# Optimization experiments

Hardware: AMD Instinct MI355X
Metric: run time of the kernel (lower is better)

Reference implementation:

```python
import jax, jax.numpy as jnp
import numpy as np

B, T, D = 2048, 200, 64
H1, H2, H3 = 256, 128, 64


def prelu(x, alpha):
    # keras PReLU default: alpha shaped like non-batch dims (T, units)
    return jnp.maximum(x, 0) + alpha * jnp.minimum(x, 0)


def setup_inputs() -> dict:
    key = jax.random.key(0)
    ks = jax.random.split(key, 12)
    q = jax.random.normal(ks[0], (B, 1, D), dtype=jnp.float32)
    k = jax.random.normal(ks[1], (B, T, D), dtype=jnp.float32)
    s1 = 1.0 / np.sqrt(4 * D)
    s2 = 1.0 / np.sqrt(H1)
    s3 = 1.0 / np.sqrt(H2)
    s4 = 1.0 / np.sqrt(H3)
    W1 = jax.random.normal(ks[2], (4 * D, H1), dtype=jnp.float32) * s1
    b1 = jnp.zeros((H1,), dtype=jnp.float32)
    a1 = jnp.full((T, H1), 0.25, dtype=jnp.float32)
    W2 = jax.random.normal(ks[3], (H1, H2), dtype=jnp.float32) * s2
    b2 = jnp.zeros((H2,), dtype=jnp.float32)
    a2 = jnp.full((T, H2), 0.25, dtype=jnp.float32)
    W3 = jax.random.normal(ks[4], (H2, H3), dtype=jnp.float32) * s3
    b3 = jnp.zeros((H3,), dtype=jnp.float32)
    a3 = jnp.full((T, H3), 0.25, dtype=jnp.float32)
    Wl = jax.random.normal(ks[5], (H3, 1), dtype=jnp.float32) * s4
    bl = jnp.zeros((1,), dtype=jnp.float32)
    return {"q": q, "k": k, "W1": W1, "b1": b1, "a1": a1,
            "W2": W2, "b2": b2, "a2": a2, "W3": W3, "b3": b3, "a3": a3,
            "Wl": Wl, "bl": bl}


def reference(q, k, W1, b1, a1, W2, b2, a2, W3, b3, a3, Wl, bl):
    # q: [B,1,D] broadcast over T; k: [B,T,D]
    qt = jnp.broadcast_to(q, k.shape)                     # [B,T,D] (tile)
    att_in = jnp.concatenate([qt, k, qt - k, qt * k], axis=-1)  # [B,T,4D]
    h = prelu(jnp.einsum('btf,fh->bth', att_in, W1) + b1, a1)   # [B,T,H1]
    h = prelu(jnp.einsum('btf,fh->bth', h, W2) + b2, a2)        # [B,T,H2]
    h = prelu(jnp.einsum('btf,fh->bth', h, W3) + b3, a3)        # [B,T,H3]
    score = (jnp.einsum('btf,fo->bto', h, Wl) + bl)[..., 0]     # [B,T]
    mask = k[:, :, 0] != 0
    score = jnp.where(mask, score, 0.0)
    out = jnp.einsum('bt,btd->bd', score, k)              # [B,D]
    return out
```

## Files before the change

### kernel.cpp

```cpp
#include <hip/hip_runtime.h>
#include <stdint.h>

#define BB 2048
#define TT 200
#define DD 64
#define FF 256
#define H1C 256
#define H2C 128
#define H3C 64

typedef __bf16 bf16x8 __attribute__((ext_vector_type(8)));
typedef float floatx16 __attribute__((ext_vector_type(16)));
typedef float f32x4 __attribute__((ext_vector_type(4)));
typedef uint32_t u32x4 __attribute__((ext_vector_type(4)));
typedef uint32_t u32x2 __attribute__((ext_vector_type(2)));
typedef unsigned short u16;
typedef u16 u16x8 __attribute__((ext_vector_type(8)));

__device__ inline u16 f2bf(float f) {
    uint32_t u = __builtin_bit_cast(uint32_t, f) + 0x8000u;
    return (u16)(u >> 16);
}
__device__ inline float bf2f(u16 h) {
    uint32_t u = ((uint32_t)h) << 16;
    return __builtin_bit_cast(float, u);
}
__device__ inline uint32_t pkbf(float lo, float hi) {
    uint32_t ul = __builtin_bit_cast(uint32_t, lo) + 0x8000u;
    uint32_t uh = __builtin_bit_cast(uint32_t, hi) + 0x8000u;
    return __builtin_amdgcn_perm(uh, ul, 0x07060302);
}

template<int K, int N>
__device__ inline void pack_w2_dev(const float* __restrict__ Wa, const float* __restrict__ Wb,
                                   float sgn, u16* __restrict__ out, int blk) {
    constexpr int NC = K / 16;
    int idx = blk * 256 + threadIdx.x;
    int j    = idx & 7;
    int lane = (idx >> 3) & 63;
    int rest = idx >> 9;
    int c  = rest % NC;
    int mt = rest / NC;
    int k = c * 16 + ((lane >> 5) << 3) + j;
    int n = mt * 32 + (lane & 31);
    out[idx] = f2bf(Wa[k * N + n] + sgn * Wb[k * N + n]);
}
template<int NTOT>
__device__ inline void pack_a_dev(const float* __restrict__ A, u16* __restrict__ out, int blk) {
    constexpr int MTOT = NTOT / 32;
    int idx = blk * 256 + threadIdx.x;
    int reg  = idx & 15;
    int lane = (idx >> 4) & 63;
    int rest = idx >> 10;
    int mt = rest % MTOT;
    int g  = rest / MTOT;
    int t  = (g >> 1) * 64 + (g & 1) * 32 + (lane & 31);
    int n  = mt * 32 + (reg & 3) + ((reg >> 2) << 3) + ((lane >> 5) << 2);
    out[idx] = (t < TT) ? f2bf(A[t * NTOT + n]) : (u16)0;
}

__global__ void pack_all(const float* __restrict__ W1, const float* __restrict__ W2,
                         const float* __restrict__ W3, const float* __restrict__ a1,
                         const float* __restrict__ a2, const float* __restrict__ a3,
                         u16* W1kdp, u16* W1pp, u16* W1qdp, u16* W2p, u16* W3p,
                         u16* A1p, u16* A2p, u16* A3p) {
    int blk = blockIdx.x;
    const float* W1q = W1;
    const float* W1k = W1 + 64 * H1C;
    const float* W1d = W1 + 128 * H1C;
    const float* W1p = W1 + 192 * H1C;
    if      (blk < 64)  pack_w2_dev<64, H1C>(W1k, W1d, -1.f, W1kdp, blk);
    else if (blk < 128) pack_w2_dev<64, H1C>(W1p, W1p,  0.f, W1pp,  blk - 64);
    else if (blk < 192) pack_w2_dev<64, H1C>(W1q, W1d,  1.f, W1qdp, blk - 128);
    else if (blk < 320) pack_w2_dev<H1C, H2C>(W2, W2,   0.f, W2p,   blk - 192);
    else if (blk < 352) pack_w2_dev<H2C, H3C>(W3, W3,   0.f, W3p,   blk - 320);
    else if (blk < 608) pack_a_dev<H1C>(a1, A1p, blk - 352);
    else if (blk < 736) pack_a_dev<H2C>(a2, A2p, blk - 608);
    else                pack_a_dev<H3C>(a3, A3p, blk - 736);
}

__device__ __attribute__((always_inline)) inline
void store_tile(u16* yrow, int S, const floatx16& acc, u16x8 av0, u16x8 av1) {
#pragma unroll
    for (int q = 0; q < 4; ++q) {
        float p[4];
#pragma unroll
        for (int i = 0; i < 4; ++i) {
            const int r = q * 4 + i;
            float v = acc[r];
            float al = bf2f(r < 8 ? av0[r] : av1[r - 8]);
            p[i] = fmaxf(v, 0.f) + al * fminf(v, 0.f);
        }
        u32x2 pw = { pkbf(p[0], p[1]), pkbf(p[2], p[3]) };
        *reinterpret_cast<u32x2*>(yrow + ((q ^ S) << 3)) = pw;
    }
}

__device__ inline void load_k4(const float* __restrict__ Kin, int b, int t, int c0,
                               f32x4* kk) {
    if (t < TT) {
        const f32x4* p = reinterpret_cast<const f32x4*>(Kin + ((size_t)b * TT + t) * DD + c0);
#pragma unroll
        for (int i = 0; i < 4; ++i) kk[i] = __builtin_nontemporal_load(p + i);
    } else {
#pragma unroll
        for (int i = 0; i < 4; ++i) kk[i] = f32x4{0.f, 0.f, 0.f, 0.f};
    }
}

__global__ __launch_bounds__(256, 2)
void attn_pool_kernel(const float* __restrict__ Q, const float* __restrict__ Kin,
                      const u16* __restrict__ W1kdp, const u16* __restrict__ W1pp,
                      const u16* __restrict__ W1qdp, const float* __restrict__ b1,
                      const u16* __restrict__ A1p,
                      const u16* __restrict__ W2p, const float* __restrict__ b2,
                      const u16* __restrict__ A2p,
                      const u16* __restrict__ W3p, const float* __restrict__ b3,
                      const u16* __restrict__ A3p,
                      const float* __restrict__ Wl, const float* __restrict__ bl,
                      float* __restrict__ Out) {
    __shared__ __align__(16) u16 k_sh[64 * 72];
    __shared__ __align__(16) u16 h1s[64 * 264];
    __shared__ __align__(16) u16 h2s[64 * 136];
    __shared__ float q_sh[64];
    __shared__ float k0_sh[64];
    __shared__ float fb1_sh[H1C];
    __shared__ float pool_red[4][64];

    const int tid  = threadIdx.x;
    const int lane = tid & 63;
    const int w    = tid >> 6;
    const int b    = blockIdx.x;
    const int tl   = lane & 31;
    const int hl   = lane >> 5;
    const int kq   = hl << 3;
    const int hsel = hl << 2;
    const int S    = (tl >> 3) & 1;
    const int r    = tid >> 2;
    const int c0   = (tid & 3) << 4;

    if (tid < 16) {
        reinterpret_cast<f32x4*>(q_sh)[tid] =
            reinterpret_cast<const f32x4*>(Q + (size_t)b * DD)[tid];
    }
    const float bl0 = bl[0];

    f32x4 kn[4];
    load_k4(Kin, b, r, c0, kn);
    __syncthreads();

    bf16x8 mf[2][4];
    {
#pragma unroll
        for (int s = 0; s < 2; ++s) {
            const int mt = w + 4 * s;
            const size_t fo = ((size_t)(mt * 4) * 64 + lane) * 8;
            floatx16 accb;
#pragma unroll
            for (int i = 0; i < 16; ++i) accb[i] = 0.f;
#pragma unroll
            for (int c = 0; c < 4; ++c) {
                u16x8 kd = *reinterpret_cast<const u16x8*>(W1kdp + fo + (size_t)c * 512);
                u16x8 pf = *reinterpret_cast<const u16x8*>(W1pp  + fo + (size_t)c * 512);
                bf16x8 qd = *reinterpret_cast<const bf16x8*>(W1qdp + fo + (size_t)c * 512);
                f32x4 qa = *reinterpret_cast<const f32x4*>(&q_sh[c * 16 + kq]);
                f32x4 qb = *reinterpret_cast<const f32x4*>(&q_sh[c * 16 + kq + 4]);
                u32x4 qpack = { pkbf(qa[0], qa[1]), pkbf(qa[2], qa[3]),
                                pkbf(qb[0], qb[1]), pkbf(qb[2], qb[3]) };
                bf16x8 qf = __builtin_bit_cast(bf16x8, qpack);
                accb = __builtin_amdgcn_mfma_f32_32x32x16_bf16(qd, qf, accb, 0, 0, 0);
                float mv[8];
#pragma unroll
                for (int j = 0; j < 4; ++j) mv[j]     = bf2f(kd[j])     + bf2f(pf[j])     * qa[j];
#pragma unroll
                for (int j = 0; j < 4; ++j) mv[4 + j] = bf2f(kd[4 + j]) + bf2f(pf[4 + j]) * qb[j];
                u32x4 mpack = { pkbf(mv[0], mv[1]), pkbf(mv[2], mv[3]),
                                pkbf(mv[4], mv[5]), pkbf(mv[6], mv[7]) };
                mf[s][c] = __builtin_bit_cast(bf16x8, mpack);
            }
            if (tl == 0) {
#pragma unroll
                for (int q = 0; q < 4; ++q) {
                    f32x4 bv = *reinterpret_cast<const f32x4*>(b1 + mt * 32 + q * 8 + hsel);
#pragma unroll
                    for (int i = 0; i < 4; ++i)
                        fb1_sh[mt * 32 + q * 8 + hsel + i] = accb[q * 4 + i] + bv[i];
                }
            }
        }
    }

    bf16x8 wf2[16];
    {
        const u16* p2 = W2p + (size_t)(w * 16) * 512 + lane * 8;
#pragma unroll
        for (int c = 0; c < 16; ++c)
            wf2[c] = *reinterpret_cast<const bf16x8*>(p2 + (size_t)c * 512);
    }
    const int mt3 = w & 1, tt3 = w >> 1;
    floatx16 bq2, bq3;
#pragma unroll
    for (int q = 0; q < 4; ++q) {
        f32x4 v2 = *reinterpret_cast<const f32x4*>(b2 + w * 32 + q * 8 + hsel);
        f32x4 v3 = *reinterpret_cast<const f32x4*>(b3 + mt3 * 32 + q * 8 + hsel);
#pragma unroll
        for (int i = 0; i < 4; ++i) { bq2[q * 4 + i] = v2[i]; bq3[q * 4 + i] = v3[i]; }
    }

    float pacc = 0.f;

#pragma unroll 1
    for (int mb = 0; mb < 4; ++mb) {
        const int t0 = mb * 64;

        {
            f32x4 kc[4] = { kn[0], kn[1], kn[2], kn[3] };
            if (mb < 3) load_k4(Kin, b, t0 + 64 + r, c0, kn);
            u32x4 ua = { pkbf(kc[0][0], kc[0][1]), pkbf(kc[0][2], kc[0][3]),
                         pkbf(kc[1][0], kc[1][1]), pkbf(kc[1][2], kc[1][3]) };
            u32x4 ub = { pkbf(kc[2][0], kc[2][1]), pkbf(kc[2][2], kc[2][3]),
                         pkbf(kc[3][0], kc[3][1]), pkbf(kc[3][2], kc[3][3]) };
            *reinterpret_cast<u32x4*>(k_sh + r * 72 + c0)     = ua;
            *reinterpret_cast<u32x4*>(k_sh + r * 72 + c0 + 8) = ub;
            if (c0 == 0) k0_sh[r] = kc[0][0];
        }
        __syncthreads();

#pragma unroll
        for (int s = 0; s < 2; ++s) {
            const int mt = w + 4 * s;
#pragma unroll
            for (int tt = 0; tt < 2; ++tt) {
                const u16* ap = A1p + (((size_t)((mb * 2 + tt) * 8 + mt) * 64 + lane) << 4);
                u16x8 av0 = *reinterpret_cast<const u16x8*>(ap);
                u16x8 av1 = *reinterpret_cast<const u16x8*>(ap + 8);
                floatx16 acc;
#pragma unroll
                for (int q = 0; q < 4; ++q) {
                    f32x4 bv = *reinterpret_cast<const f32x4*>(&fb1_sh[mt * 32 + q * 8 + hsel]);
#pragma unroll
                    for (int i = 0; i < 4; ++i) acc[q * 4 + i] = bv[i];
                }
                const u16* xb = k_sh + (tt * 32 + tl) * 72 + kq;
#pragma unroll
                for (int c = 0; c < 4; ++c)
                    acc = __builtin_amdgcn_mfma_f32_32x32x16_bf16(
                        mf[s][c], *reinterpret_cast<const bf16x8*>(xb + c * 16), acc, 0, 0, 0);
                store_tile(h1s + (tt * 32 + tl) * 264 + mt * 32 + hsel, S, acc, av0, av1);
            }
        }
        __syncthreads();

#pragma unroll
        for (int tt = 0; tt < 2; ++tt) {
            const u16* ap = A2p + (((size_t)((mb * 2 + tt) * 4 + w) * 64 + lane) << 4);
            u16x8 av0 = *reinterpret_cast<const u16x8*>(ap);
            u16x8 av1 = *reinterpret_cast<const u16x8*>(ap + 8);
            floatx16 acc = bq2;
            const u16* xb = h1s + (tt * 32 + tl) * 264 + ((hl ^ S) << 3);
#pragma unroll
            for (int c = 0; c < 16; ++c)
                acc = __builtin_amdgcn_mfma_f32_32x32x16_bf16(
                    wf2[c], *reinterpret_cast<const bf16x8*>(xb + c * 16), acc, 0, 0, 0);
            store_tile(h2s + (tt * 32 + tl) * 136 + w * 32 + hsel, S, acc, av0, av1);
        }
        __syncthreads();

        {
            const u16* ap = A3p + (((size_t)((mb * 2 + tt3) * 2 + mt3) * 64 + lane) << 4);
            u16x8 av0 = *reinterpret_cast<const u16x8*>(ap);
            u16x8 av1 = *reinterpret_cast<const u16x8*>(ap + 8);
            const u16* wp3 = W3p + (size_t)(mt3 * 8) * 512 + lane * 8;
            floatx16 acc = bq3;
            const u16* xb = h2s + (tt3 * 32 + tl) * 136 + ((hl ^ S) << 3);
#pragma unroll
            for (int c = 0; c < 8; ++c)
                acc = __builtin_amdgcn_mfma_f32_32x32x16_bf16(
                    *reinterpret_cast<const bf16x8*>(wp3 + (size_t)c * 512),
                    *reinterpret_cast<const bf16x8*>(xb + c * 16), acc, 0, 0, 0);
            store_tile(h1s + (tt3 * 32 + tl) * 264 + mt3 * 32 + hsel, S, acc, av0, av1);
        }
        __syncthreads();

        {
            const int sr  = tid >> 2;
            const int p   = tid & 3;
            const int Ssc = (sr >> 3) & 1;
            const u16* hrow = h1s + sr * 264 + p * 16;
            u16x8 hv0 = *reinterpret_cast<const u16x8*>(hrow + 8 * Ssc);
            u16x8 hv1 = *reinterpret_cast<const u16x8*>(hrow + 8 * (1 - Ssc));
            float s = 0.f;
#pragma unroll
            for (int i = 0; i < 8; ++i) s += bf2f(hv0[i]) * Wl[p * 16 + i];
#pragma unroll
            for (int i = 0; i < 8; ++i) s += bf2f(hv1[i]) * Wl[p * 16 + 8 + i];
            s += __shfl_xor(s, 1);
            s += __shfl_xor(s, 2);
            const int t = t0 + sr;
            float sc = s + bl0;
            if (t >= TT || k0_sh[sr] == 0.f) sc = 0.f;
#pragma unroll
            for (int i = 0; i < 16; ++i) {
                float si = __shfl(sc, 4 * i);
                pacc += si * bf2f(k_sh[(w * 16 + i) * 72 + lane]);
            }
        }
        __syncthreads();
    }

    pool_red[w][lane] = pacc;
    __syncthreads();
    if (tid < 64) {
        Out[(size_t)b * DD + tid] = pool_red[0][tid] + pool_red[1][tid]
                                  + pool_red[2][tid] + pool_red[3][tid];
    }
}

extern "C" void kernel_launch(void* const* d_in, const int* in_sizes, int n_in,
                              void* d_out, int out_size, void* d_ws, size_t ws_size,
                              hipStream_t stream) {
    (void)in_sizes; (void)n_in; (void)out_size; (void)ws_size;
    const float* Q  = (const float*)d_in[0];
    const float* Kk = (const float*)d_in[1];
    const float* W1 = (const float*)d_in[2];
    const float* b1 = (const float*)d_in[3];
    const float* a1 = (const float*)d_in[4];
    const float* W2 = (const float*)d_in[5];
    const float* b2 = (const float*)d_in[6];
    const float* a2 = (const float*)d_in[7];
    const float* W3 = (const float*)d_in[8];
    const float* b3 = (const float*)d_in[9];
    const float* a3 = (const float*)d_in[10];
    const float* Wl = (const float*)d_in[11];
    const float* bl = (const float*)d_in[12];
    float* Out = (float*)d_out;

    u16* ws    = (u16*)d_ws;
    u16* W1kdp = ws;
    u16* W1pp  = W1kdp + 16384;
    u16* W1qdp = W1pp  + 16384;
    u16* W2p   = W1qdp + 16384;
    u16* W3p   = W2p   + 32768;
    u16* A1p   = W3p   + 8192;
    u16* A2p   = A1p   + 65536;
    u16* A3p   = A2p   + 32768;

    hipLaunchKernelGGL(pack_all, dim3(800), dim3(256), 0, stream,
                       W1, W2, W3, a1, a2, a3,
                       W1kdp, W1pp, W1qdp, W2p, W3p, A1p, A2p, A3p);
    hipLaunchKernelGGL(attn_pool_kernel, dim3(BB), dim3(256), 0, stream,
                       Q, Kk, W1kdp, W1pp, W1qdp, b1, A1p, W2p, b2, A2p,
                       W3p, b3, A3p, Wl, bl, Out);
}
```

Measured before the change: 306.6 us.

## Halve time-tile to 32 rows, double-buffer K, raise occupancy to 3 blocks

Processes the sequence in 8 tiles of 32 timesteps instead of 4 tiles of 64, which halves the shared-memory buffers and register footprint so launch bounds can target 3 blocks per CU. K staging is double-buffered, which lets the trailing barrier of each iteration be removed. A new 4-way XOR swizzle replaces the 2-way one to reduce LDS bank conflicts, and biases are staged in shared memory. The trade-off is more loop iterations and barriers per unit of work, and layer 3 now runs on only half the waves.

```diff
diff --git a/kernel.cpp b/kernel.cpp
--- a/kernel.cpp
+++ b/kernel.cpp
@@ -30,6 +30,7 @@
     uint32_t uh = __builtin_bit_cast(uint32_t, hi) + 0x8000u;
     return __builtin_amdgcn_perm(uh, ul, 0x07060302);
 }
+__device__ inline int swzf(int row) { return (row >> 3) & 3; }
 
 template<int K, int N>
 __device__ inline void pack_w2_dev(const float* __restrict__ Wa, const float* __restrict__ Wb,
@@ -54,7 +55,7 @@
     int rest = idx >> 10;
     int mt = rest % MTOT;
     int g  = rest / MTOT;
-    int t  = (g >> 1) * 64 + (g & 1) * 32 + (lane & 31);
+    int t  = g * 32 + (lane & 31);
     int n  = mt * 32 + (reg & 3) + ((reg >> 2) << 3) + ((lane >> 5) << 2);
     out[idx] = (t < TT) ? f2bf(A[t * NTOT + n]) : (u16)0;
 }
@@ -96,19 +97,19 @@
     }
 }
 
-__device__ inline void load_k4(const float* __restrict__ Kin, int b, int t, int c0,
-                               f32x4* kk) {
+__device__ inline void load_k2(const float* __restrict__ Kin, int b, int t, int c0,
+                               f32x4& a, f32x4& c) {
     if (t < TT) {
         const f32x4* p = reinterpret_cast<const f32x4*>(Kin + ((size_t)b * TT + t) * DD + c0);
-#pragma unroll
-        for (int i = 0; i < 4; ++i) kk[i] = __builtin_nontemporal_load(p + i);
+        a = __builtin_nontemporal_load(p);
+        c = __builtin_nontemporal_load(p + 1);
     } else {
-#pragma unroll
-        for (int i = 0; i < 4; ++i) kk[i] = f32x4{0.f, 0.f, 0.f, 0.f};
-    }
-}
-
-__global__ __launch_bounds__(256, 2)
+        a = f32x4{0.f, 0.f, 0.f, 0.f};
+        c = f32x4{0.f, 0.f, 0.f, 0.f};
+    }
+}
+
+__global__ __launch_bounds__(256, 3)
 void attn_pool_kernel(const float* __restrict__ Q, const float* __restrict__ Kin,
                       const u16* __restrict__ W1kdp, const u16* __restrict__ W1pp,
                       const u16* __restrict__ W1qdp, const float* __restrict__ b1,
@@ -119,12 +120,14 @@
                       const u16* __restrict__ A3p,
                       const float* __restrict__ Wl, const float* __restrict__ bl,
                       float* __restrict__ Out) {
-    __shared__ __align__(16) u16 k_sh[64 * 72];
-    __shared__ __align__(16) u16 h1s[64 * 264];
-    __shared__ __align__(16) u16 h2s[64 * 136];
+    __shared__ __align__(16) u16 k_sh[2][32 * 72];
+    __shared__ __align__(16) u16 h1s[32 * 264];
+    __shared__ __align__(16) u16 h2s[32 * 136];
     __shared__ float q_sh[64];
-    __shared__ float k0_sh[64];
+    __shared__ float k0_sh[2][32];
     __shared__ float fb1_sh[H1C];
+    __shared__ float b2_sh[H2C];
+    __shared__ float b3_sh[H3C];
     __shared__ float pool_red[4][64];
 
     const int tid  = threadIdx.x;
@@ -135,57 +138,58 @@
     const int hl   = lane >> 5;
     const int kq   = hl << 3;
     const int hsel = hl << 2;
-    const int S    = (tl >> 3) & 1;
-    const int r    = tid >> 2;
-    const int c0   = (tid & 3) << 4;
+    const int swzv = swzf(tl);
+    const int r    = tid >> 3;
+    const int g    = tid & 7;
+    const int c0   = g << 3;
 
     if (tid < 16) {
         reinterpret_cast<f32x4*>(q_sh)[tid] =
             reinterpret_cast<const f32x4*>(Q + (size_t)b * DD)[tid];
     }
+    if (tid < H2C) b2_sh[tid] = b2[tid];
+    if (tid < H3C) b3_sh[tid] = b3[tid];
     const float bl0 = bl[0];
 
-    f32x4 kn[4];
-    load_k4(Kin, b, r, c0, kn);
+    f32x4 kn0, kn1;
+    load_k2(Kin, b, r, c0, kn0, kn1);
     __syncthreads();
 
     bf16x8 mf[2][4];
-    {
-#pragma unroll
-        for (int s = 0; s < 2; ++s) {
-            const int mt = w + 4 * s;
-            const size_t fo = ((size_t)(mt * 4) * 64 + lane) * 8;
-            floatx16 accb;
-#pragma unroll
-            for (int i = 0; i < 16; ++i) accb[i] = 0.f;
-#pragma unroll
-            for (int c = 0; c < 4; ++c) {
-                u16x8 kd = *reinterpret_cast<const u16x8*>(W1kdp + fo + (size_t)c * 512);
-                u16x8 pf = *reinterpret_cast<const u16x8*>(W1pp  + fo + (size_t)c * 512);
-                bf16x8 qd = *reinterpret_cast<const bf16x8*>(W1qdp + fo + (size_t)c * 512);
-                f32x4 qa = *reinterpret_cast<const f32x4*>(&q_sh[c * 16 + kq]);
-                f32x4 qb = *reinterpret_cast<const f32x4*>(&q_sh[c * 16 + kq + 4]);
-                u32x4 qpack = { pkbf(qa[0], qa[1]), pkbf(qa[2], qa[3]),
-                                pkbf(qb[0], qb[1]), pkbf(qb[2], qb[3]) };
-                bf16x8 qf = __builtin_bit_cast(bf16x8, qpack);
-                accb = __builtin_amdgcn_mfma_f32_32x32x16_bf16(qd, qf, accb, 0, 0, 0);
-                float mv[8];
-#pragma unroll
-                for (int j = 0; j < 4; ++j) mv[j]     = bf2f(kd[j])     + bf2f(pf[j])     * qa[j];
-#pragma unroll
-                for (int j = 0; j < 4; ++j) mv[4 + j] = bf2f(kd[4 + j]) + bf2f(pf[4 + j]) * qb[j];
-                u32x4 mpack = { pkbf(mv[0], mv[1]), pkbf(mv[2], mv[3]),
-                                pkbf(mv[4], mv[5]), pkbf(mv[6], mv[7]) };
-                mf[s][c] = __builtin_bit_cast(bf16x8, mpack);
-            }
-            if (tl == 0) {
-#pragma unroll
-                for (int q = 0; q < 4; ++q) {
-                    f32x4 bv = *reinterpret_cast<const f32x4*>(b1 + mt * 32 + q * 8 + hsel);
-#pragma unroll
-                    for (int i = 0; i < 4; ++i)
-                        fb1_sh[mt * 32 + q * 8 + hsel + i] = accb[q * 4 + i] + bv[i];
-                }
+#pragma unroll
+    for (int s = 0; s < 2; ++s) {
+        const int mt = w + 4 * s;
+        const size_t fo = ((size_t)(mt * 4) * 64 + lane) * 8;
+        floatx16 accb;
+#pragma unroll
+        for (int i = 0; i < 16; ++i) accb[i] = 0.f;
+#pragma unroll
+        for (int c = 0; c < 4; ++c) {
+            u16x8 kd = *reinterpret_cast<const u16x8*>(W1kdp + fo + (size_t)c * 512);
+            u16x8 pf = *reinterpret_cast<const u16x8*>(W1pp  + fo + (size_t)c * 512);
+            bf16x8 qd = *reinterpret_cast<const bf16x8*>(W1qdp + fo + (size_t)c * 512);
+            f32x4 qa = *reinterpret_cast<const f32x4*>(&q_sh[c * 16 + kq]);
+            f32x4 qb = *reinterpret_cast<const f32x4*>(&q_sh[c * 16 + kq + 4]);
+            u32x4 qpack = { pkbf(qa[0], qa[1]), pkbf(qa[2], qa[3]),
+                            pkbf(qb[0], qb[1]), pkbf(qb[2], qb[3]) };
+            bf16x8 qf = __builtin_bit_cast(bf16x8, qpack);
+            accb = __builtin_amdgcn_mfma_f32_32x32x16_bf16(qd, qf, accb, 0, 0, 0);
+            float mv[8];
+#pragma unroll
+            for (int j = 0; j < 4; ++j) mv[j]     = bf2f(kd[j])     + bf2f(pf[j])     * qa[j];
+#pragma unroll
+            for (int j = 0; j < 4; ++j) mv[4 + j] = bf2f(kd[4 + j]) + bf2f(pf[4 + j]) * qb[j];
+            u32x4 mpack = { pkbf(mv[0], mv[1]), pkbf(mv[2], mv[3]),
+                            pkbf(mv[4], mv[5]), pkbf(mv[6], mv[7]) };
+            mf[s][c] = __builtin_bit_cast(bf16x8, mpack);
+        }
+        if (tl == 0) {
+#pragma unroll
+            for (int q = 0; q < 4; ++q) {
+                f32x4 bv = *reinterpret_cast<const f32x4*>(b1 + mt * 32 + q * 8 + hsel);
+#pragma unroll
+                for (int i = 0; i < 4; ++i)
+                    fb1_sh[mt * 32 + q * 8 + hsel + i] = accb[q * 4 + i] + bv[i];
             }
         }
     }
@@ -197,115 +201,119 @@
         for (int c = 0; c < 16; ++c)
             wf2[c] = *reinterpret_cast<const bf16x8*>(p2 + (size_t)c * 512);
     }
-    const int mt3 = w & 1, tt3 = w >> 1;
-    floatx16 bq2, bq3;
-#pragma unroll
-    for (int q = 0; q < 4; ++q) {
-        f32x4 v2 = *reinterpret_cast<const f32x4*>(b2 + w * 32 + q * 8 + hsel);
-        f32x4 v3 = *reinterpret_cast<const f32x4*>(b3 + mt3 * 32 + q * 8 + hsel);
-#pragma unroll
-        for (int i = 0; i < 4; ++i) { bq2[q * 4 + i] = v2[i]; bq3[q * 4 + i] = v3[i]; }
-    }
 
     float pacc = 0.f;
 
 #pragma unroll 1
-    for (int mb = 0; mb < 4; ++mb) {
-        const int t0 = mb * 64;
+    for (int mb = 0; mb < 8; ++mb) {
+        const int t0  = mb * 32;
+        const int buf = mb & 1;
+        u16* ksh = k_sh[buf];
 
         {
-            f32x4 kc[4] = { kn[0], kn[1], kn[2], kn[3] };
-            if (mb < 3) load_k4(Kin, b, t0 + 64 + r, c0, kn);
-            u32x4 ua = { pkbf(kc[0][0], kc[0][1]), pkbf(kc[0][2], kc[0][3]),
-                         pkbf(kc[1][0], kc[1][1]), pkbf(kc[1][2], kc[1][3]) };
-            u32x4 ub = { pkbf(kc[2][0], kc[2][1]), pkbf(kc[2][2], kc[2][3]),
-                         pkbf(kc[3][0], kc[3][1]), pkbf(kc[3][2], kc[3][3]) };
-            *reinterpret_cast<u32x4*>(k_sh + r * 72 + c0)     = ua;
-            *reinterpret_cast<u32x4*>(k_sh + r * 72 + c0 + 8) = ub;
-            if (c0 == 0) k0_sh[r] = kc[0][0];
+            f32x4 kc0 = kn0, kc1 = kn1;
+            if (mb < 7) load_k2(Kin, b, t0 + 32 + r, c0, kn0, kn1);
+            u32x4 uk = { pkbf(kc0[0], kc0[1]), pkbf(kc0[2], kc0[3]),
+                         pkbf(kc1[0], kc1[1]), pkbf(kc1[2], kc1[3]) };
+            *reinterpret_cast<u32x4*>(ksh + r * 72 + ((g ^ swzf(r)) << 3)) = uk;
+            if (g == 0) k0_sh[buf][r] = kc0[0];
         }
         __syncthreads();
 
 #pragma unroll
         for (int s = 0; s < 2; ++s) {
             const int mt = w + 4 * s;
-#pragma unroll
-            for (int tt = 0; tt < 2; ++tt) {
-                const u16* ap = A1p + (((size_t)((mb * 2 + tt) * 8 + mt) * 64 + lane) << 4);
-                u16x8 av0 = *reinterpret_cast<const u16x8*>(ap);
-                u16x8 av1 = *reinterpret_cast<const u16x8*>(ap + 8);
-                floatx16 acc;
-#pragma unroll
-                for (int q = 0; q < 4; ++q) {
-                    f32x4 bv = *reinterpret_cast<const f32x4*>(&fb1_sh[mt * 32 + q * 8 + hsel]);
-#pragma unroll
-                    for (int i = 0; i < 4; ++i) acc[q * 4 + i] = bv[i];
-                }
-                const u16* xb = k_sh + (tt * 32 + tl) * 72 + kq;
-#pragma unroll
-                for (int c = 0; c < 4; ++c)
-                    acc = __builtin_amdgcn_mfma_f32_32x32x16_bf16(
-                        mf[s][c], *reinterpret_cast<const bf16x8*>(xb + c * 16), acc, 0, 0, 0);
-                store_tile(h1s + (tt * 32 + tl) * 264 + mt * 32 + hsel, S, acc, av0, av1);
-            }
-        }
-        __syncthreads();
-
-#pragma unroll
-        for (int tt = 0; tt < 2; ++tt) {
-            const u16* ap = A2p + (((size_t)((mb * 2 + tt) * 4 + w) * 64 + lane) << 4);
+            const u16* ap = A1p + (((size_t)(mb * 8 + mt) * 64 + lane) << 4);
             u16x8 av0 = *reinterpret_cast<const u16x8*>(ap);
             u16x8 av1 = *reinterpret_cast<const u16x8*>(ap + 8);
-            floatx16 acc = bq2;
-            const u16* xb = h1s + (tt * 32 + tl) * 264 + ((hl ^ S) << 3);
+            floatx16 acc;
+#pragma unroll
+            for (int q = 0; q < 4; ++q) {
+                f32x4 bv = *reinterpret_cast<const f32x4*>(&fb1_sh[mt * 32 + q * 8 + hsel]);
+#pragma unroll
+                for (int i = 0; i < 4; ++i) acc[q * 4 + i] = bv[i];
+            }
+            const u16* xb = ksh + tl * 72;
+#pragma unroll
+            for (int c = 0; c < 4; ++c)
+                acc = __builtin_amdgcn_mfma_f32_32x32x16_bf16(
+                    mf[s][c],
+                    *reinterpret_cast<const bf16x8*>(xb + (((2 * c + hl) ^ swzv) << 3)),
+                    acc, 0, 0, 0);
+            store_tile(h1s + tl * 264 + mt * 32 + hsel, swzv, acc, av0, av1);
+        }
+        __syncthreads();
+
+        {
+            const u16* ap = A2p + (((size_t)(mb * 4 + w) * 64 + lane) << 4);
+            u16x8 av0 = *reinterpret_cast<const u16x8*>(ap);
+            u16x8 av1 = *reinterpret_cast<const u16x8*>(ap + 8);
+            floatx16 acc;
+#pragma unroll
+            for (int q = 0; q < 4; ++q) {
+                f32x4 bv = *reinterpret_cast<const f32x4*>(&b2_sh[w * 32 + q * 8 + hsel]);
+#pragma unroll
+                for (int i = 0; i < 4; ++i) acc[q * 4 + i] = bv[i];
+            }
+            const u16* xb = h1s + tl * 264;
 #pragma unroll
             for (int c = 0; c < 16; ++c)
                 acc = __builtin_amdgcn_mfma_f32_32x32x16_bf16(
-                    wf2[c], *reinterpret_cast<const bf16x8*>(xb + c * 16), acc, 0, 0, 0);
-            store_tile(h2s + (tt * 32 + tl) * 136 + w * 32 + hsel, S, acc, av0, av1);
+                    wf2[c],
+                    *reinterpret_cast<const bf16x8*>(xb + (((2 * c + hl) ^ swzv) << 3)),
+                    acc, 0, 0, 0);
+            store_tile(h2s + tl * 136 + w * 32 + hsel, swzv, acc, av0, av1);
         }
         __syncthreads();
 
-        {
-            const u16* ap = A3p + (((size_t)((mb * 2 + tt3) * 2 + mt3) * 64 + lane) << 4);
+        if (w < 2) {
+            const u16* ap = A3p + (((size_t)(mb * 2 + w) * 64 + lane) << 4);
             u16x8 av0 = *reinterpret_cast<const u16x8*>(ap);
             u16x8 av1 = *reinterpret_cast<const u16x8*>(ap + 8);
-            const u16* wp3 = W3p + (size_t)(mt3 * 8) * 512 + lane * 8;
-            floatx16 acc = bq3;
-            const u16* xb = h2s + (tt3 * 32 + tl) * 136 + ((hl ^ S) << 3);
+            const u16* wp3 = W3p + (size_t)(w * 8) * 512 + lane * 8;
+            floatx16 acc;
+#pragma unroll
+            for (int q = 0; q < 4; ++q) {
+                f32x4 bv = *reinterpret_cast<const f32x4*>(&b3_sh[w * 32 + q * 8 + hsel]);
+#pragma unroll
+                for (int i = 0; i < 4; ++i) acc[q * 4 + i] = bv[i];
+            }
+            const u16* xb = h2s + tl * 136;
 #pragma unroll
             for (int c = 0; c < 8; ++c)
                 acc = __builtin_amdgcn_mfma_f32_32x32x16_bf16(
                     *reinterpret_cast<const bf16x8*>(wp3 + (size_t)c * 512),
-                    *reinterpret_cast<const bf16x8*>(xb + c * 16), acc, 0, 0, 0);
-            store_tile(h1s + (tt3 * 32 + tl) * 264 + mt3 * 32 + hsel, S, acc, av0, av1);
+                    *reinterpret_cast<const bf16x8*>(xb + (((2 * c + hl) ^ swzv) << 3)),
+                    acc, 0, 0, 0);
+            store_tile(h1s + tl * 264 + w * 32 + hsel, swzv, acc, av0, av1);
         }
         __syncthreads();
 
         {
-            const int sr  = tid >> 2;
-            const int p   = tid & 3;
-            const int Ssc = (sr >> 3) & 1;
-            const u16* hrow = h1s + sr * 264 + p * 16;
-            u16x8 hv0 = *reinterpret_cast<const u16x8*>(hrow + 8 * Ssc);
-            u16x8 hv1 = *reinterpret_cast<const u16x8*>(hrow + 8 * (1 - Ssc));
+            const int sr = tid >> 3;
+            const int p  = tid & 7;
+            const int ss = swzf(sr);
+            u16x8 hv = *reinterpret_cast<const u16x8*>(h1s + sr * 264 + ((p ^ ss) << 3));
+            const f32x4 wl0 = *reinterpret_cast<const f32x4*>(Wl + p * 8);
+            const f32x4 wl1 = *reinterpret_cast<const f32x4*>(Wl + p * 8 + 4);
             float s = 0.f;
 #pragma unroll
-            for (int i = 0; i < 8; ++i) s += bf2f(hv0[i]) * Wl[p * 16 + i];
-#pragma unroll
-            for (int i = 0; i < 8; ++i) s += bf2f(hv1[i]) * Wl[p * 16 + 8 + i];
+            for (int i = 0; i < 4; ++i) s += bf2f(hv[i]) * wl0[i];
+#pragma unroll
+            for (int i = 0; i < 4; ++i) s += bf2f(hv[4 + i]) * wl1[i];
             s += __shfl_xor(s, 1);
             s += __shfl_xor(s, 2);
+            s += __shfl_xor(s, 4);
             const int t = t0 + sr;
             float sc = s + bl0;
-            if (t >= TT || k0_sh[sr] == 0.f) sc = 0.f;
-#pragma unroll
-            for (int i = 0; i < 16; ++i) {
-                float si = __shfl(sc, 4 * i);
-                pacc += si * bf2f(k_sh[(w * 16 + i) * 72 + lane]);
-            }
-        }
-        __syncthreads();
+            if (t >= TT || k0_sh[buf][sr] == 0.f) sc = 0.f;
+#pragma unroll
+            for (int i = 0; i < 8; ++i) {
+                const int row = w * 8 + i;
+                float si = __shfl(sc, 8 * i);
+                pacc += si * bf2f(ksh[row * 72 + (((lane >> 3) ^ swzf(row)) << 3) + (lane & 7)]);
+            }
+        }
     }
 
     pool_red[w][lane] = pacc;
```

New measurement: 445.9 us. 1.45x slower.

## Restructure MLP stages: double-buffer K tile, fuse final projection, split accumulators

Applied to the files above, without the earlier changes.

The K tile and mask buffer are double-buffered, which lets the trailing barrier of each time block be dropped. The K tile is stored with an XOR swizzle, and layer 1 now loads the K fragments once and shares them across both output tiles. Layers 2 and 3 split their MFMA chains into two independent accumulators to shorten dependency chains, and layer-2 activations are software-prefetched. W3 and the biases are now kept in registers and LDS. The final Wl projection is fused into the layer-3 epilogue so h3 is no longer written to LDS and read back, at the cost of more registers and a cross-wave score reduction through LDS.

```diff
diff --git a/kernel.cpp b/kernel.cpp
--- a/kernel.cpp
+++ b/kernel.cpp
@@ -54,7 +54,7 @@
     int rest = idx >> 10;
     int mt = rest % MTOT;
     int g  = rest / MTOT;
-    int t  = (g >> 1) * 64 + (g & 1) * 32 + (lane & 31);
+    int t  = g * 32 + (lane & 31);
     int n  = mt * 32 + (reg & 3) + ((reg >> 2) << 3) + ((lane >> 5) << 2);
     out[idx] = (t < TT) ? f2bf(A[t * NTOT + n]) : (u16)0;
 }
@@ -80,14 +80,15 @@
 }
 
 __device__ __attribute__((always_inline)) inline
-void store_tile(u16* yrow, int S, const floatx16& acc, u16x8 av0, u16x8 av1) {
+void store_tile(u16* yrow, int S, const floatx16& accA, const floatx16& accB,
+                u16x8 av0, u16x8 av1) {
 #pragma unroll
     for (int q = 0; q < 4; ++q) {
         float p[4];
 #pragma unroll
         for (int i = 0; i < 4; ++i) {
             const int r = q * 4 + i;
-            float v = acc[r];
+            float v = accA[r] + accB[r];
             float al = bf2f(r < 8 ? av0[r] : av1[r - 8]);
             p[i] = fmaxf(v, 0.f) + al * fminf(v, 0.f);
         }
@@ -119,12 +120,15 @@
                       const u16* __restrict__ A3p,
                       const float* __restrict__ Wl, const float* __restrict__ bl,
                       float* __restrict__ Out) {
-    __shared__ __align__(16) u16 k_sh[64 * 72];
+    __shared__ __align__(16) u16 k_sh[2][64 * 72];
     __shared__ __align__(16) u16 h1s[64 * 264];
     __shared__ __align__(16) u16 h2s[64 * 136];
     __shared__ float q_sh[64];
-    __shared__ float k0_sh[64];
+    __shared__ float k0_sh[2][64];
     __shared__ float fb1_sh[H1C];
+    __shared__ float b2_sh[H2C];
+    __shared__ float b3_sh[H3C];
+    __shared__ float scorep[2][64];
     __shared__ float pool_red[4][64];
 
     const int tid  = threadIdx.x;
@@ -138,11 +142,14 @@
     const int S    = (tl >> 3) & 1;
     const int r    = tid >> 2;
     const int c0   = (tid & 3) << 4;
+    const int Sr   = (r >> 3) & 1;
 
     if (tid < 16) {
         reinterpret_cast<f32x4*>(q_sh)[tid] =
             reinterpret_cast<const f32x4*>(Q + (size_t)b * DD)[tid];
     }
+    if (tid < H2C) b2_sh[tid] = b2[tid];
+    if (tid < H3C) b3_sh[tid] = b3[tid];
     const float bl0 = bl[0];
 
     f32x4 kn[4];
@@ -150,68 +157,64 @@
     __syncthreads();
 
     bf16x8 mf[2][4];
-    {
-#pragma unroll
-        for (int s = 0; s < 2; ++s) {
-            const int mt = w + 4 * s;
-            const size_t fo = ((size_t)(mt * 4) * 64 + lane) * 8;
-            floatx16 accb;
-#pragma unroll
-            for (int i = 0; i < 16; ++i) accb[i] = 0.f;
-#pragma unroll
-            for (int c = 0; c < 4; ++c) {
-                u16x8 kd = *reinterpret_cast<const u16x8*>(W1kdp + fo + (size_t)c * 512);
-                u16x8 pf = *reinterpret_cast<const u16x8*>(W1pp  + fo + (size_t)c * 512);
-                bf16x8 qd = *reinterpret_cast<const bf16x8*>(W1qdp + fo + (size_t)c * 512);
-                f32x4 qa = *reinterpret_cast<const f32x4*>(&q_sh[c * 16 + kq]);
-                f32x4 qb = *reinterpret_cast<const f32x4*>(&q_sh[c * 16 + kq + 4]);
-                u32x4 qpack = { pkbf(qa[0], qa[1]), pkbf(qa[2], qa[3]),
-                                pkbf(qb[0], qb[1]), pkbf(qb[2], qb[3]) };
-                bf16x8 qf = __builtin_bit_cast(bf16x8, qpack);
-                accb = __builtin_amdgcn_mfma_f32_32x32x16_bf16(qd, qf, accb, 0, 0, 0);
-                float mv[8];
-#pragma unroll
-                for (int j = 0; j < 4; ++j) mv[j]     = bf2f(kd[j])     + bf2f(pf[j])     * qa[j];
-#pragma unroll
-                for (int j = 0; j < 4; ++j) mv[4 + j] = bf2f(kd[4 + j]) + bf2f(pf[4 + j]) * qb[j];
-                u32x4 mpack = { pkbf(mv[0], mv[1]), pkbf(mv[2], mv[3]),
-                                pkbf(mv[4], mv[5]), pkbf(mv[6], mv[7]) };
-                mf[s][c] = __builtin_bit_cast(bf16x8, mpack);
-            }
-            if (tl == 0) {
-#pragma unroll
-                for (int q = 0; q < 4; ++q) {
-                    f32x4 bv = *reinterpret_cast<const f32x4*>(b1 + mt * 32 + q * 8 + hsel);
-#pragma unroll
-                    for (int i = 0; i < 4; ++i)
-                        fb1_sh[mt * 32 + q * 8 + hsel + i] = accb[q * 4 + i] + bv[i];
-                }
-            }
-        }
-    }
-
-    bf16x8 wf2[16];
+#pragma unroll
+    for (int s = 0; s < 2; ++s) {
+        const int mt = w + 4 * s;
+        const size_t fo = ((size_t)(mt * 4) * 64 + lane) * 8;
+        floatx16 accb;
+#pragma unroll
+        for (int i = 0; i < 16; ++i) accb[i] = 0.f;
+#pragma unroll
+        for (int c = 0; c < 4; ++c) {
+            u16x8 kd = *reinterpret_cast<const u16x8*>(W1kdp + fo + (size_t)c * 512);
+            u16x8 pf = *reinterpret_cast<const u16x8*>(W1pp  + fo + (size_t)c * 512);
+            bf16x8 qd = *reinterpret_cast<const bf16x8*>(W1qdp + fo + (size_t)c * 512);
+            f32x4 qa = *reinterpret_cast<const f32x4*>(&q_sh[c * 16 + kq]);
+            f32x4 qb = *reinterpret_cast<const f32x4*>(&q_sh[c * 16 + kq + 4]);
+            u32x4 qpack = { pkbf(qa[0], qa[1]), pkbf(qa[2], qa[3]),
+                            pkbf(qb[0], qb[1]), pkbf(qb[2], qb[3]) };
+            bf16x8 qf = __builtin_bit_cast(bf16x8, qpack);
+            accb = __builtin_amdgcn_mfma_f32_32x32x16_bf16(qd, qf, accb, 0, 0, 0);
+            float mv[8];
+#pragma unroll
+            for (int j = 0; j < 4; ++j) mv[j]     = bf2f(kd[j])     + bf2f(pf[j])     * qa[j];
+#pragma unroll
+            for (int j = 0; j < 4; ++j) mv[4 + j] = bf2f(kd[4 + j]) + bf2f(pf[4 + j]) * qb[j];
+            u32x4 mpack = { pkbf(mv[0], mv[1]), pkbf(mv[2], mv[3]),
+                            pkbf(mv[4], mv[5]), pkbf(mv[6], mv[7]) };
+            mf[s][c] = __builtin_bit_cast(bf16x8, mpack);
+        }
+        if (tl == 0) {
+#pragma unroll
+            for (int q = 0; q < 4; ++q) {
+                f32x4 bv = *reinterpret_cast<const f32x4*>(b1 + mt * 32 + q * 8 + hsel);
+#pragma unroll
+                for (int i = 0; i < 4; ++i)
+                    fb1_sh[mt * 32 + q * 8 + hsel + i] = accb[q * 4 + i] + bv[i];
+            }
+        }
+    }
+
+    const int mt3 = w & 1, tt3 = w >> 1;
+    bf16x8 wf2[16], wf3[8];
     {
         const u16* p2 = W2p + (size_t)(w * 16) * 512 + lane * 8;
 #pragma unroll
         for (int c = 0; c < 16; ++c)
             wf2[c] = *reinterpret_cast<const bf16x8*>(p2 + (size_t)c * 512);
-    }
-    const int mt3 = w & 1, tt3 = w >> 1;
-    floatx16 bq2, bq3;
-#pragma unroll
-    for (int q = 0; q < 4; ++q) {
-        f32x4 v2 = *reinterpret_cast<const f32x4*>(b2 + w * 32 + q * 8 + hsel);
-        f32x4 v3 = *reinterpret_cast<const f32x4*>(b3 + mt3 * 32 + q * 8 + hsel);
-#pragma unroll
-        for (int i = 0; i < 4; ++i) { bq2[q * 4 + i] = v2[i]; bq3[q * 4 + i] = v3[i]; }
+        const u16* p3 = W3p + (size_t)(mt3 * 8) * 512 + lane * 8;
+#pragma unroll
+        for (int c = 0; c < 8; ++c)
+            wf3[c] = *reinterpret_cast<const bf16x8*>(p3 + (size_t)c * 512);
     }
 
     float pacc = 0.f;
 
 #pragma unroll 1
     for (int mb = 0; mb < 4; ++mb) {
-        const int t0 = mb * 64;
+        const int t0  = mb * 64;
+        const int buf = mb & 1;
+        u16* ksh = k_sh[buf];
 
         {
             f32x4 kc[4] = { kn[0], kn[1], kn[2], kn[3] };
@@ -220,34 +223,43 @@
                          pkbf(kc[1][0], kc[1][1]), pkbf(kc[1][2], kc[1][3]) };
             u32x4 ub = { pkbf(kc[2][0], kc[2][1]), pkbf(kc[2][2], kc[2][3]),
                          pkbf(kc[3][0], kc[3][1]), pkbf(kc[3][2], kc[3][3]) };
-            *reinterpret_cast<u32x4*>(k_sh + r * 72 + c0)     = ua;
-            *reinterpret_cast<u32x4*>(k_sh + r * 72 + c0 + 8) = ub;
-            if (c0 == 0) k0_sh[r] = kc[0][0];
+            *reinterpret_cast<u32x4*>(ksh + r * 72 + (c0 ^ (Sr << 3)))       = ua;
+            *reinterpret_cast<u32x4*>(ksh + r * 72 + ((c0 + 8) ^ (Sr << 3))) = ub;
+            if (c0 == 0) k0_sh[buf][r] = kc[0][0];
         }
         __syncthreads();
 
 #pragma unroll
-        for (int s = 0; s < 2; ++s) {
-            const int mt = w + 4 * s;
-#pragma unroll
-            for (int tt = 0; tt < 2; ++tt) {
-                const u16* ap = A1p + (((size_t)((mb * 2 + tt) * 8 + mt) * 64 + lane) << 4);
-                u16x8 av0 = *reinterpret_cast<const u16x8*>(ap);
-                u16x8 av1 = *reinterpret_cast<const u16x8*>(ap + 8);
-                floatx16 acc;
-#pragma unroll
-                for (int q = 0; q < 4; ++q) {
-                    f32x4 bv = *reinterpret_cast<const f32x4*>(&fb1_sh[mt * 32 + q * 8 + hsel]);
-#pragma unroll
-                    for (int i = 0; i < 4; ++i) acc[q * 4 + i] = bv[i];
+        for (int tt = 0; tt < 2; ++tt) {
+            const u16* ap0 = A1p + (((size_t)((mb * 2 + tt) * 8 + w) * 64 + lane) << 4);
+            const u16* ap1 = A1p + (((size_t)((mb * 2 + tt) * 8 + w + 4) * 64 + lane) << 4);
+            u16x8 av00 = *reinterpret_cast<const u16x8*>(ap0);
+            u16x8 av01 = *reinterpret_cast<const u16x8*>(ap0 + 8);
+            u16x8 av10 = *reinterpret_cast<const u16x8*>(ap1);
+            u16x8 av11 = *reinterpret_cast<const u16x8*>(ap1 + 8);
+            const u16* xb = ksh + (tt * 32 + tl) * 72 + ((hl ^ S) << 3);
+            bf16x8 kf[4];
+#pragma unroll
+            for (int c = 0; c < 4; ++c)
+                kf[c] = *reinterpret_cast<const bf16x8*>(xb + c * 16);
+            floatx16 acc0, acc1, zz;
+#pragma unroll
+            for (int q = 0; q < 4; ++q) {
+                f32x4 b0 = *reinterpret_cast<const f32x4*>(&fb1_sh[w * 32 + q * 8 + hsel]);
+                f32x4 b1v = *reinterpret_cast<const f32x4*>(&fb1_sh[(w + 4) * 32 + q * 8 + hsel]);
+#pragma unroll
+                for (int i = 0; i < 4; ++i) {
+                    acc0[q * 4 + i] = b0[i]; acc1[q * 4 + i] = b1v[i]; zz[q * 4 + i] = 0.f;
                 }
-                const u16* xb = k_sh + (tt * 32 + tl) * 72 + kq;
-#pragma unroll
-                for (int c = 0; c < 4; ++c)
-                    acc = __builtin_amdgcn_mfma_f32_32x32x16_bf16(
-                        mf[s][c], *reinterpret_cast<const bf16x8*>(xb + c * 16), acc, 0, 0, 0);
-                store_tile(h1s + (tt * 32 + tl) * 264 + mt * 32 + hsel, S, acc, av0, av1);
-            }
+            }
+#pragma unroll
+            for (int c = 0; c < 4; ++c) {
+                acc0 = __builtin_amdgcn_mfma_f32_32x32x16_bf16(mf[0][c], kf[c], acc0, 0, 0, 0);
+                acc1 = __builtin_amdgcn_mfma_f32_32x32x16_bf16(mf[1][c], kf[c], acc1, 0, 0, 0);
+            }
+            u16* yr = h1s + (tt * 32 + tl) * 264;
+            store_tile(yr + w * 32 + hsel, S, acc0, zz, av00, av01);
+            store_tile(yr + (w + 4) * 32 + hsel, S, acc1, zz, av10, av11);
         }
         __syncthreads();
 
@@ -256,13 +268,41 @@
             const u16* ap = A2p + (((size_t)((mb * 2 + tt) * 4 + w) * 64 + lane) << 4);
             u16x8 av0 = *reinterpret_cast<const u16x8*>(ap);
             u16x8 av1 = *reinterpret_cast<const u16x8*>(ap + 8);
-            floatx16 acc = bq2;
             const u16* xb = h1s + (tt * 32 + tl) * 264 + ((hl ^ S) << 3);
-#pragma unroll
-            for (int c = 0; c < 16; ++c)
-                acc = __builtin_amdgcn_mfma_f32_32x32x16_bf16(
-                    wf2[c], *reinterpret_cast<const bf16x8*>(xb + c * 16), acc, 0, 0, 0);
-            store_tile(h2s + (tt * 32 + tl) * 136 + w * 32 + hsel, S, acc, av0, av1);
+            floatx16 accA, accB;
+#pragma unroll
+            for (int q = 0; q < 4; ++q) {
+                f32x4 bv = *reinterpret_cast<const f32x4*>(&b2_sh[w * 32 + q * 8 + hsel]);
+#pragma unroll
+                for (int i = 0; i < 4; ++i) { accA[q * 4 + i] = bv[i]; accB[q * 4 + i] = 0.f; }
+            }
+            bf16x8 cur[4];
+#pragma unroll
+            for (int c = 0; c < 4; ++c)
+                cur[c] = *reinterpret_cast<const bf16x8*>(xb + c * 16);
+#pragma unroll
+            for (int g = 0; g < 4; ++g) {
+                bf16x8 nxt[4];
+                if (g < 3) {
+#pragma unroll
+                    for (int c = 0; c < 4; ++c)
+                        nxt[c] = *reinterpret_cast<const bf16x8*>(xb + ((g + 1) * 4 + c) * 16);
+                }
+                if (g & 1) {
+#pragma unroll
+                    for (int c = 0; c < 4; ++c)
+                        accB = __builtin_amdgcn_mfma_f32_32x32x16_bf16(wf2[g * 4 + c], cur[c], accB, 0, 0, 0);
+                } else {
+#pragma unroll
+                    for (int c = 0; c < 4; ++c)
+                        accA = __builtin_amdgcn_mfma_f32_32x32x16_bf16(wf2[g * 4 + c], cur[c], accA, 0, 0, 0);
+                }
+                if (g < 3) {
+#pragma unroll
+                    for (int c = 0; c < 4; ++c) cur[c] = nxt[c];
+                }
+            }
+            store_tile(h2s + (tt * 32 + tl) * 136 + w * 32 + hsel, S, accA, accB, av0, av1);
         }
         __syncthreads();
 
@@ -270,42 +310,58 @@
             const u16* ap = A3p + (((size_t)((mb * 2 + tt3) * 2 + mt3) * 64 + lane) << 4);
             u16x8 av0 = *reinterpret_cast<const u16x8*>(ap);
             u16x8 av1 = *reinterpret_cast<const u16x8*>(ap + 8);
-            const u16* wp3 = W3p + (size_t)(mt3 * 8) * 512 + lane * 8;
-            floatx16 acc = bq3;
+            f32x4 wlq[4];
+#pragma unroll
+            for (int q = 0; q < 4; ++q)
+                wlq[q] = *reinterpret_cast<const f32x4*>(Wl + mt3 * 32 + q * 8 + hsel);
             const u16* xb = h2s + (tt3 * 32 + tl) * 136 + ((hl ^ S) << 3);
-#pragma unroll
-            for (int c = 0; c < 8; ++c)
-                acc = __builtin_amdgcn_mfma_f32_32x32x16_bf16(
-                    *reinterpret_cast<const bf16x8*>(wp3 + (size_t)c * 512),
-                    *reinterpret_cast<const bf16x8*>(xb + c * 16), acc, 0, 0, 0);
-            store_tile(h1s + (tt3 * 32 + tl) * 264 + mt3 * 32 + hsel, S, acc, av0, av1);
+            floatx16 accA, accB;
+#pragma unroll
+            for (int q = 0; q < 4; ++q) {
+                f32x4 bv = *reinterpret_cast<const f32x4*>(&b3_sh[mt3 * 32 + q * 8 + hsel]);
+#pragma unroll
+                for (int i = 0; i < 4; ++i) { accA[q * 4 + i] = bv[i]; accB[q * 4 + i] = 0.f; }
+            }
+            bf16x8 cur[4], nxt[4];
+#pragma unroll
+            for (int c = 0; c < 4; ++c)
+                cur[c] = *reinterpret_cast<const bf16x8*>(xb + c * 16);
+#pragma unroll
+            for (int c = 0; c < 4; ++c)
+                nxt[c] = *reinterpret_cast<const bf16x8*>(xb + (4 + c) * 16);
+#pragma unroll
+            for (int c = 0; c < 4; ++c) {
+                accA = __builtin_amdgcn_mfma_f32_32x32x16_bf16(wf3[c], cur[c], accA, 0, 0, 0);
+                accB = __builtin_amdgcn_mfma_f32_32x32x16_bf16(wf3[4 + c], nxt[c], accB, 0, 0, 0);
+            }
+            float s = 0.f;
+#pragma unroll
+            for (int q = 0; q < 4; ++q) {
+#pragma unroll
+                for (int i = 0; i < 4; ++i) {
+                    const int rr = q * 4 + i;
+                    float v = accA[rr] + accB[rr];
+                    float al = bf2f(rr < 8 ? av0[rr] : av1[rr - 8]);
+                    float p = fmaxf(v, 0.f) + al * fminf(v, 0.f);
+                    s += p * wlq[q][i];
+                }
+            }
+            s += __shfl_xor(s, 32);
+            if (hl == 0) scorep[mt3][tt3 * 32 + tl] = s;
         }
         __syncthreads();
 
         {
-            const int sr  = tid >> 2;
-            const int p   = tid & 3;
-            const int Ssc = (sr >> 3) & 1;
-            const u16* hrow = h1s + sr * 264 + p * 16;
-            u16x8 hv0 = *reinterpret_cast<const u16x8*>(hrow + 8 * Ssc);
-            u16x8 hv1 = *reinterpret_cast<const u16x8*>(hrow + 8 * (1 - Ssc));
-            float s = 0.f;
-#pragma unroll
-            for (int i = 0; i < 8; ++i) s += bf2f(hv0[i]) * Wl[p * 16 + i];
-#pragma unroll
-            for (int i = 0; i < 8; ++i) s += bf2f(hv1[i]) * Wl[p * 16 + 8 + i];
-            s += __shfl_xor(s, 1);
-            s += __shfl_xor(s, 2);
-            const int t = t0 + sr;
-            float sc = s + bl0;
-            if (t >= TT || k0_sh[sr] == 0.f) sc = 0.f;
+            float sc_l = scorep[0][lane] + scorep[1][lane] + bl0;
+            const int t = t0 + lane;
+            if (t >= TT || k0_sh[buf][lane] == 0.f) sc_l = 0.f;
 #pragma unroll
             for (int i = 0; i < 16; ++i) {
-                float si = __shfl(sc, 4 * i);
-                pacc += si * bf2f(k_sh[(w * 16 + i) * 72 + lane]);
-            }
-        }
-        __syncthreads();
+                const int row = w * 16 + i;
+                float si = __shfl(sc_l, row);
+                pacc += si * bf2f(ksh[row * 72 + (lane ^ (((row >> 3) & 1) << 3))]);
+            }
+        }
     }
 
     pool_red[w][lane] = pacc;
```

Result: no change. 307.2 us (+0.2%).
